# Kernel optimization log

Hardware: AMD Instinct MI355X
Metric: run time of the kernel (lower is better)

The kernel has to match this reference:

```python
import jax, jax.numpy as jnp
import numpy as np

B, S, HID = 1, 4096, 2048
NH, NKV, HD = 8, 4, 256
SCALING = 256.0 ** -0.5
SOFT_CAP = 50.0
WINDOW = 4096
ROPE_THETA = 10000.0
NEG = jnp.finfo(jnp.float32).min


def _build_mask():
    q = np.arange(S)[:, None]
    k = np.arange(S)[None, :]
    causal = k <= q
    windowed = (q - k) < WINDOW
    allowed = causal & windowed
    m = np.where(allowed, 0.0, np.finfo(np.float32).min).astype(np.float32)
    return jnp.asarray(m)[None, None]  # [1,1,S,S]


def setup_inputs() -> dict:
    key = jax.random.key(0)
    ks = jax.random.split(key, 5)
    scale = 0.02
    return {
        "hidden_states": jax.random.normal(ks[0], (B, S, HID), jnp.float32),
        "attention_mask": _build_mask(),
        "position_ids": jnp.arange(S, dtype=jnp.int64)[None, :],
        "wq": jax.random.normal(ks[1], (HID, NH * HD), jnp.float32) * scale,
        "wk": jax.random.normal(ks[2], (HID, NKV * HD), jnp.float32) * scale,
        "wv": jax.random.normal(ks[3], (HID, NKV * HD), jnp.float32) * scale,
        "wo": jax.random.normal(ks[4], (NH * HD, HID), jnp.float32) * scale,
    }


def _rope(position_ids):
    inv_freq = 1.0 / (ROPE_THETA ** (jnp.arange(0, HD, 2, dtype=jnp.float32) / HD))
    freqs = position_ids.astype(jnp.float32)[:, :, None] * inv_freq[None, None, :]  # [B,S,HD/2]
    emb = jnp.concatenate([freqs, freqs], axis=-1)  # [B,S,HD]
    return jnp.cos(emb), jnp.sin(emb)


def _rotate_half(x):
    x1, x2 = x[..., : HD // 2], x[..., HD // 2 :]
    return jnp.concatenate([-x2, x1], axis=-1)


def _attn(hidden_states, attention_mask, position_ids, wq, wk, wv, wo):
    bsz, q_len, _ = hidden_states.shape
    q = (hidden_states @ wq).reshape(bsz, q_len, NH, HD).transpose(0, 2, 1, 3)    # [B,NH,S,HD]
    k = (hidden_states @ wk).reshape(bsz, q_len, NKV, HD).transpose(0, 2, 1, 3)   # [B,NKV,S,HD]
    v = (hidden_states @ wv).reshape(bsz, q_len, NKV, HD).transpose(0, 2, 1, 3)
    cos, sin = _rope(position_ids)
    cos, sin = cos[:, None], sin[:, None]  # [B,1,S,HD]
    q = q * cos + _rotate_half(q) * sin
    k = k * cos + _rotate_half(k) * sin
    n_rep = NH // NKV
    k = jnp.repeat(k, n_rep, axis=1)  # [B,NH,S,HD]
    v = jnp.repeat(v, n_rep, axis=1)
    scores = jnp.einsum("bhqd,bhkd->bhqk", q, k) * SCALING
    scores = jnp.tanh(scores / SOFT_CAP) * SOFT_CAP
    scores = scores + attention_mask
    probs = jax.nn.softmax(scores.astype(jnp.float32), axis=-1).astype(q.dtype)
    out = jnp.einsum("bhqk,bhkd->bhqd", probs, v)  # [B,NH,S,HD]
    out = out.transpose(0, 2, 1, 3).reshape(bsz, q_len, NH * HD)
    return out @ wo


def reference(hidden_states, attention_mask, position_ids, wq, wk, wv, wo):
    return _attn(hidden_states, attention_mask, position_ids, wq, wk, wv, wo)
```

## Files before the change

### kernel.cpp

```cpp
#include <hip/hip_runtime.h>


#define SEQ 4096
#define HIDDEN 2048
#define NHEADS 8
#define HDIM 256

typedef unsigned short u16;
typedef __attribute__((ext_vector_type(8))) __bf16 bf16x8;
typedef __attribute__((ext_vector_type(4))) float f32x4;
typedef __attribute__((ext_vector_type(16))) float f32x16;

static __device__ inline u16 f2bf(float f) {
  union { float f; unsigned u; } x; x.f = f;
  unsigned r = x.u + 0x7FFFu + ((x.u >> 16) & 1u);
  return (u16)(r >> 16);
}
static __device__ inline float bf2f(u16 u) {
  union { unsigned u; float f; } x; x.u = ((unsigned)u) << 16;
  return x.f;
}

typedef __attribute__((address_space(1))) const unsigned int* gp_t;
typedef __attribute__((address_space(3))) unsigned int* lp_t;
static __device__ inline void load_lds16(const u16* g, u16* l) {
  __builtin_amdgcn_global_load_lds((gp_t)g, (lp_t)l, 16, 0, 0);
}


__global__ void convert_hs_kernel(const float* __restrict__ src, u16* __restrict__ dst) {
  int i = blockIdx.x * 256 + threadIdx.x;
  float4 v = ((const float4*)src)[i];
  ushort4 o;
  o.x = f2bf(v.x); o.y = f2bf(v.y); o.z = f2bf(v.z); o.w = f2bf(v.w);
  ((ushort4*)dst)[i] = o;
}

__global__ void transpose_w_kernel(const float* __restrict__ src, u16* __restrict__ dst,
                                   int K, int N) {
  __shared__ u16 tile[64][65];
  int n0 = blockIdx.x * 64, k0 = blockIdx.y * 64;
  int tid = threadIdx.x;
  for (int i = 0; i < 16; i++) {
    int idx = i * 256 + tid; int r = idx >> 6, c = idx & 63;
    tile[r][c] = f2bf(src[(size_t)(k0 + r) * N + n0 + c]);
  }
  __syncthreads();
  for (int i = 0; i < 16; i++) {
    int idx = i * 256 + tid; int r = idx >> 6, c = idx & 63;
    dst[(size_t)(n0 + r) * K + k0 + c] = tile[c][r];
  }
}

__global__ void rope_kernel(u16* qkv) {
  int idx = blockIdx.x * 256 + threadIdx.x;
  int s = idx / (12 * 128);
  int rem = idx - s * (12 * 128);
  int head = rem >> 7;
  int i = rem & 127;
  float inv = __expf(-(float)i * 0.0719557841560639f);
  float ang = (float)s * inv;
  float sn, cs;
  sincosf(ang, &sn, &cs);
  size_t base = (size_t)s * 4096 + head * 256 + i;
  float a = bf2f(qkv[base]);
  float b = bf2f(qkv[base + 128]);
  qkv[base]       = f2bf(a * cs - b * sn);
  qkv[base + 128] = f2bf(b * cs + a * sn);
}

__global__ void transpose_v_kernel(const u16* __restrict__ qkv, u16* __restrict__ vT) {
  __shared__ u16 tile[64][65];
  int d0 = blockIdx.x * 64, s0 = blockIdx.y * 64;
  int tid = threadIdx.x;
  for (int i = 0; i < 16; i++) {
    int idx = i * 256 + tid; int r = idx >> 6, c = idx & 63;
    tile[r][c] = qkv[(size_t)(s0 + r) * 4096 + 3072 + d0 + c];
  }
  __syncthreads();
  for (int i = 0; i < 16; i++) {
    int idx = i * 256 + tid; int r = idx >> 6, c = idx & 63;
    vT[(size_t)(d0 + r) * 4096 + s0 + c] = tile[c][r];
  }
}


template <bool OUT_F32>
__global__ __launch_bounds__(256, 2) void gemm_bf16_kernel(
    const u16* __restrict__ A, const u16* __restrict__ Bt, void* __restrict__ Cout,
    int M, int N, int K) {
  __shared__ __attribute__((aligned(16))) u16 As[128 * 64];
  __shared__ __attribute__((aligned(16))) u16 Bs[128 * 64];
  int tid = threadIdx.x;
  int wave = tid >> 6, lane = tid & 63;
  int lm = lane & 15, qd = lane >> 4;
  int m0 = blockIdx.y * 128, n0 = blockIdx.x * 128;
  int wm = (wave >> 1) * 64, wn = (wave & 1) * 64;

  f32x4 acc[4][4];
#pragma unroll
  for (int a = 0; a < 4; a++)
#pragma unroll
    for (int b = 0; b < 4; b++) acc[a][b] = (f32x4){0.f, 0.f, 0.f, 0.f};

  int srow = lane >> 3;
  int scol = (lane & 7) * 8;

  for (int kt = 0; kt < K; kt += 64) {
    __syncthreads();
#pragma unroll
    for (int t = 0; t < 4; t++) {
      int j = wave * 4 + t;
      int row = j * 8 + srow;
      load_lds16(A  + (size_t)(m0 + row) * K + kt + scol, As + j * 512);
      load_lds16(Bt + (size_t)(n0 + row) * K + kt + scol, Bs + j * 512);
    }
    __syncthreads();
#pragma unroll
    for (int kk = 0; kk < 2; kk++) {
      bf16x8 af[4], bfr[4];
#pragma unroll
      for (int mi = 0; mi < 4; mi++)
        af[mi] = *(const bf16x8*)&As[(wm + mi * 16 + lm) * 64 + kk * 32 + qd * 8];
#pragma unroll
      for (int ni = 0; ni < 4; ni++)
        bfr[ni] = *(const bf16x8*)&Bs[(wn + ni * 16 + lm) * 64 + kk * 32 + qd * 8];
#pragma unroll
      for (int mi = 0; mi < 4; mi++)
#pragma unroll
        for (int ni = 0; ni < 4; ni++)
          acc[mi][ni] = __builtin_amdgcn_mfma_f32_16x16x32_bf16(af[mi], bfr[ni],
                                                               acc[mi][ni], 0, 0, 0);
    }
  }
#pragma unroll
  for (int mi = 0; mi < 4; mi++) {
    int row = m0 + wm + mi * 16 + qd * 4;
#pragma unroll
    for (int ni = 0; ni < 4; ni++) {
      int col = n0 + wn + ni * 16 + lm;
#pragma unroll
      for (int r = 0; r < 4; r++) {
        float v = acc[mi][ni][r];
        if (OUT_F32) ((float*)Cout)[(size_t)(row + r) * N + col] = v;
        else         ((u16*)Cout)[(size_t)(row + r) * N + col] = f2bf(v);
      }
    }
  }
}


__global__ __launch_bounds__(256, 2) void flash_kernel(
    const u16* __restrict__ qkv, const u16* __restrict__ vT,
    u16* __restrict__ attn, float* __restrict__ PA, float* __restrict__ PB,
    float* __restrict__ lbuf ) {
  __shared__ __attribute__((aligned(16))) u16 Ks[64 * 256];
  __shared__ __attribute__((aligned(16))) u16 Vs[256 * 64];
  __shared__ __attribute__((aligned(16))) u16 Pl[64 * 64];

  int tid = threadIdx.x;
  int w = tid >> 6, lane = tid & 63;
  int l31 = lane & 31, hi = lane >> 5;
  int qhalf = w >> 1, kh = w & 1, dhalf = w & 1;

  int b = blockIdx.x;
  int r = b & 255;
  int h = r & 7;
  int pi = r >> 3;
  int kvh = h >> 1;
  int isA = (b < 256);
  int nseg = isA ? 2 : 1;

  int vlc = (lane & 7) ^ ((lane >> 3) & 7);
  int vro = lane >> 3;

  const u16* Kg  = qkv + 2048 + (size_t)kvh * 256;
  const u16* Vg0 = vT + (size_t)(kvh * 256) * 4096;

  bf16x8 ones;
#pragma unroll
  for (int e = 0; e < 8; e++) ones[e] = (__bf16)1.0f;

  for (int si = 0; si < nseg; si++) {
    int qt, k0, k1, mode;
    if (isA && si == 0) { qt = pi;      k0 = 0;       k1 = pi + 1;  mode = 0; }
    else if (isA)       { qt = 63 - pi; k0 = 0;       k1 = 31 - pi; mode = 1; }
    else                { qt = 63 - pi; k0 = 31 - pi; k1 = 64 - pi; mode = 2; }

    {
      const u16* Qg = qkv + (size_t)(qt * 64) * 4096 + h * 256;
#pragma unroll
      for (int s = 0; s < 8; s++) {
        int kr = (w * 8 + s) * 2 + hi;
        int klc = l31 ^ (kr & 31);
        load_lds16(Qg + (size_t)kr * 4096 + klc * 8, &Ks[(w * 8 + s) * 512]);
      }
    }
    __syncthreads();

    bf16x8 aq[16];
#pragma unroll
    for (int kc = 0; kc < 16; kc++)
      aq[kc] = *(const bf16x8*)&Ks[(qhalf * 32 + l31) * 256 +
                                   (((kc * 2 + hi) ^ l31) << 3)];
    __syncthreads();

    f32x16 ao[4];
#pragma unroll
    for (int g = 0; g < 4; g++) ao[g] = (f32x16)(0.f);
    f32x16 al = (f32x16)(0.f);

    for (int t = k0; t < k1; t++) {
      {
        const u16* Kt = Kg + (size_t)(t * 64) * 4096;
        const u16* Vt = Vg0 + t * 64;
#pragma unroll
        for (int s = 0; s < 8; s++) {
          int kr = (w * 8 + s) * 2 + hi;
          int klc = l31 ^ (kr & 31);
          load_lds16(Kt + (size_t)kr * 4096 + klc * 8, &Ks[(w * 8 + s) * 512]);
          int vr = (w * 8 + s) * 8 + vro;
          load_lds16(Vt + (size_t)vr * 4096 + vlc * 8, &Vs[(w * 8 + s) * 512]);
        }
      }
      __syncthreads();

      f32x16 se = (f32x16)(0.f);
      f32x16 so = (f32x16)(0.f);
#pragma unroll
      for (int kc = 0; kc < 8; kc++) {
        bf16x8 bk0 = *(const bf16x8*)&Ks[(kh * 32 + l31) * 256 +
                                         ((((2 * kc) * 2 + hi) ^ l31) << 3)];
        se = __builtin_amdgcn_mfma_f32_32x32x16_bf16(aq[2 * kc], bk0, se, 0, 0, 0);
        bf16x8 bk1 = *(const bf16x8*)&Ks[(kh * 32 + l31) * 256 +
                                         ((((2 * kc + 1) * 2 + hi) ^ l31) << 3)];
        so = __builtin_amdgcn_mfma_f32_32x32x16_bf16(aq[2 * kc + 1], bk1, so, 0, 0, 0);
      }
      f32x16 sacc = se + so;

      bool diag = (t == qt);
#pragma unroll
      for (int reg = 0; reg < 16; reg++) {
        int qa = 4 * hi + 8 * (reg >> 2) + (reg & 3);
        int q64 = qhalf * 32 + qa;
        int key64 = kh * 32 + l31;
        float x = sacc[reg] * 0.00125f;
        float x2 = x * x;
        float th = x * (1.f + x2 * (-0.33333333f + x2 * 0.13333333f));
        float p = exp2f(72.134752f * (th - 1.f));
        if (diag && key64 > q64) p = 0.f;
        Pl[q64 * 64 + (((key64 >> 3) ^ (q64 & 7)) << 3) + (key64 & 7)] = f2bf(p);
      }
      __syncthreads();

      bf16x8 ap[4];
#pragma unroll
      for (int kc = 0; kc < 4; kc++)
        ap[kc] = *(const bf16x8*)&Pl[(qhalf * 32 + l31) * 64 +
                                     (((kc * 2 + hi) ^ (l31 & 7)) << 3)];
#pragma unroll
      for (int g = 0; g < 4; g++) {
        int dd = dhalf * 128 + g * 32 + l31;
#pragma unroll
        for (int kc = 0; kc < 4; kc++) {
          bf16x8 bv = *(const bf16x8*)&Vs[dd * 64 +
                                          (((kc * 2 + hi) ^ (l31 & 7)) << 3)];
          ao[g] = __builtin_amdgcn_mfma_f32_32x32x16_bf16(ap[kc], bv, ao[g], 0, 0, 0);
        }
      }
#pragma unroll
      for (int kc = 0; kc < 4; kc++)
        al = __builtin_amdgcn_mfma_f32_32x32x16_bf16(ap[kc], ones, al, 0, 0, 0);

      __syncthreads();
    }

    if (mode == 0) {
      float inv_l[16];
#pragma unroll
      for (int reg = 0; reg < 16; reg++) inv_l[reg] = 1.f / al[reg];
      int qs = qt * 64 + qhalf * 32;
#pragma unroll
      for (int g = 0; g < 4; g++) {
        int col = h * 256 + dhalf * 128 + g * 32 + l31;
#pragma unroll
        for (int reg = 0; reg < 16; reg++) {
          int row = qs + 4 * hi + 8 * (reg >> 2) + (reg & 3);
          attn[(size_t)row * 2048 + col] = f2bf(ao[g][reg] * inv_l[reg]);
        }
      }
    } else {
      float* Pbuf = (mode == 1) ? PA : PB;
#pragma unroll
      for (int g = 0; g < 4; g++) {
        int col = dhalf * 128 + g * 32 + l31;
#pragma unroll
        for (int reg = 0; reg < 16; reg++) {
          int row = qhalf * 32 + 4 * hi + 8 * (reg >> 2) + (reg & 3);
          Pbuf[((size_t)r * 64 + row) * 256 + col] = ao[g][reg];
        }
      }
      if (dhalf == 0 && l31 == 0) {
        size_t lbase = (size_t)(r * 16 + (mode - 1)) * 2048 + 1536;
#pragma unroll
        for (int reg = 0; reg < 16; reg++) {
          int row = qhalf * 32 + 4 * hi + 8 * (reg >> 2) + (reg & 3);
          lbuf[lbase + row] = al[reg];
        }
      }
    }
  }
}

__global__ __launch_bounds__(256) void combine_kernel(
    const float* __restrict__ PA, const float* __restrict__ PB,
    const float* __restrict__ lbuf, u16* __restrict__ attn) {
  int p = blockIdx.x;
  int h = p & 7, pi = p >> 3;
  int qt2 = 63 - pi;
  int tid = threadIdx.x;
  int row = tid >> 2;
  int c0 = (tid & 3) * 64;
  float la = lbuf[(size_t)(p * 16) * 2048 + 1536 + row];
  float lb = lbuf[(size_t)(p * 16 + 1) * 2048 + 1536 + row];
  float inv = 1.f / (la + lb);
  size_t src = ((size_t)p * 64 + row) * 256 + c0;
  size_t dst = (size_t)(qt2 * 64 + row) * 2048 + h * 256 + c0;
#pragma unroll
  for (int c = 0; c < 64; c += 4) {
    float4 a = *(const float4*)&PA[src + c];
    float4 bb = *(const float4*)&PB[src + c];
    ushort4 o;
    o.x = f2bf((a.x + bb.x) * inv);
    o.y = f2bf((a.y + bb.y) * inv);
    o.z = f2bf((a.z + bb.z) * inv);
    o.w = f2bf((a.w + bb.w) * inv);
    *(ushort4*)&attn[dst + c] = o;
  }
}


extern "C" void kernel_launch(void* const* d_in, const int* in_sizes, int n_in,
                              void* d_out, int out_size, void* d_ws, size_t ws_size,
                              hipStream_t stream) {
  const float* hs = (const float*)d_in[0];
  const float* wq = (const float*)d_in[3];
  const float* wk = (const float*)d_in[4];
  const float* wv = (const float*)d_in[5];
  const float* wo = (const float*)d_in[6];
  float* out = (float*)d_out;

  char* ws = (char*)d_ws;
  u16* hsb    = (u16*)(ws);
  u16* wqkvT  = (u16*)(ws + 16777216);
  u16* woT    = (u16*)(ws + 33554432);
  u16* qkv    = (u16*)(ws + 41943040);
  u16* vT     = (u16*)(ws + 75497472);
  u16* attn   = (u16*)(ws + 83886080);
  float* PA   = (float*)(ws);
  float* PB   = (float*)(ws + 16777216);
  float* lbuf = (float*)(ws + 41943040);

  convert_hs_kernel<<<8192, 256, 0, stream>>>(hs, hsb);
  transpose_w_kernel<<<dim3(32, 32), 256, 0, stream>>>(wq, wqkvT, HIDDEN, 2048);
  transpose_w_kernel<<<dim3(16, 32), 256, 0, stream>>>(wk, wqkvT + (size_t)2048 * HIDDEN, HIDDEN, 1024);
  transpose_w_kernel<<<dim3(16, 32), 256, 0, stream>>>(wv, wqkvT + (size_t)3072 * HIDDEN, HIDDEN, 1024);
  transpose_w_kernel<<<dim3(32, 32), 256, 0, stream>>>(wo, woT, HIDDEN, 2048);

  gemm_bf16_kernel<false><<<dim3(32, 32), 256, 0, stream>>>(hsb, wqkvT, qkv, 4096, 4096, 2048);
  rope_kernel<<<24576, 256, 0, stream>>>(qkv);
  transpose_v_kernel<<<dim3(16, 64), 256, 0, stream>>>(qkv, vT);

  flash_kernel<<<512, 256, 0, stream>>>(qkv, vT, attn, PA, PB, lbuf);
  combine_kernel<<<256, 256, 0, stream>>>(PA, PB, lbuf, attn);
  gemm_bf16_kernel<true><<<dim3(16, 32), 256, 0, stream>>>(attn, woT, out, 4096, 2048, 2048);
}
```

Baseline: 482.6 us.

## Add 256x256-tile pipelined GEMM for the fused QKV projection

```diff
diff --git a/kernel.cpp b/kernel.cpp
--- a/kernel.cpp
+++ b/kernel.cpp
@@ -26,6 +26,8 @@
 static __device__ inline void load_lds16(const u16* g, u16* l) {
   __builtin_amdgcn_global_load_lds((gp_t)g, (lp_t)l, 16, 0, 0);
 }
+
+#define BARX() do { __builtin_amdgcn_s_barrier(); asm volatile("" ::: "memory"); } while (0)
 
 
 __global__ void convert_hs_kernel(const float* __restrict__ src, u16* __restrict__ dst) {
@@ -85,6 +87,110 @@
 }
 
 
+__global__ __launch_bounds__(512, 2) void gemm256_kernel(
+    const u16* __restrict__ A, const u16* __restrict__ Bt, u16* __restrict__ C,
+    int M, int N, int K) {
+  __shared__ __attribute__((aligned(16))) u16 lds[4][2][256 * 32];
+  int tid = threadIdx.x;
+  int wid = tid >> 6, lane = tid & 63;
+  int lm = lane & 15, kq = lane >> 4;
+  int wm = (wid >> 2) * 128, wn = (wid & 3) * 64;
+  int m0 = blockIdx.y * 256, n0 = blockIdx.x * 256;
+  int T = K >> 5;
+
+  int idx0 = tid, idx1 = 512 + tid;
+  int r0 = idx0 >> 2, c0 = idx0 & 3;
+  int r1 = idx1 >> 2, c1 = idx1 & 3;
+  const u16* gA0 = A  + (size_t)(m0 + r0) * K + ((c0 ^ (r0 & 3)) << 3);
+  const u16* gA1 = A  + (size_t)(m0 + r1) * K + ((c1 ^ (r1 & 3)) << 3);
+  const u16* gB0 = Bt + (size_t)(n0 + r0) * K + ((c0 ^ (r0 & 3)) << 3);
+  const u16* gB1 = Bt + (size_t)(n0 + r1) * K + ((c1 ^ (r1 & 3)) << 3);
+
+  f32x4 acc[8][4];
+#pragma unroll
+  for (int a = 0; a < 8; a++)
+#pragma unroll
+    for (int b = 0; b < 4; b++) acc[a][b] = (f32x4){0.f, 0.f, 0.f, 0.f};
+
+  int xsw = ((kq ^ (lm & 3)) << 3);
+
+#pragma unroll
+  for (int t = 0; t < 2; t++) {
+    int s = t & 3;
+    load_lds16(gA0 + t * 32, &lds[s][0][idx0 * 8]);
+    load_lds16(gA1 + t * 32, &lds[s][0][idx1 * 8]);
+    load_lds16(gB0 + t * 32, &lds[s][1][idx0 * 8]);
+    load_lds16(gB1 + t * 32, &lds[s][1][idx1 * 8]);
+  }
+  asm volatile("s_waitcnt vmcnt(4)" ::: "memory");
+  BARX();
+
+  for (int t = 0; t < T; ++t) {
+    const u16* As = &lds[t & 3][0][0];
+    const u16* Bs = &lds[t & 3][1][0];
+    int sn = (t + 2) & 3;
+    bool st = (t + 2) < T;
+
+    bf16x8 a0[4], bb[4];
+#pragma unroll
+    for (int f = 0; f < 4; f++)
+      a0[f] = *(const bf16x8*)&As[(wm + f * 16 + lm) * 32 + xsw];
+#pragma unroll
+    for (int f = 0; f < 4; f++)
+      bb[f] = *(const bf16x8*)&Bs[(wn + f * 16 + lm) * 32 + xsw];
+    if (st) {
+      load_lds16(gA0 + (t + 2) * 32, &lds[sn][0][idx0 * 8]);
+      load_lds16(gA1 + (t + 2) * 32, &lds[sn][0][idx1 * 8]);
+    }
+    BARX();
+    __builtin_amdgcn_s_setprio(1);
+#pragma unroll
+    for (int mi = 0; mi < 4; mi++)
+#pragma unroll
+      for (int ni = 0; ni < 4; ni++)
+        acc[mi][ni] = __builtin_amdgcn_mfma_f32_16x16x32_bf16(a0[mi], bb[ni],
+                                                             acc[mi][ni], 0, 0, 0);
+    __builtin_amdgcn_s_setprio(0);
+
+    bf16x8 a1[4];
+#pragma unroll
+    for (int f = 0; f < 4; f++)
+      a1[f] = *(const bf16x8*)&As[(wm + 64 + f * 16 + lm) * 32 + xsw];
+    if (st) {
+      load_lds16(gB0 + (t + 2) * 32, &lds[sn][1][idx0 * 8]);
+      load_lds16(gB1 + (t + 2) * 32, &lds[sn][1][idx1 * 8]);
+    }
+    BARX();
+    __builtin_amdgcn_s_setprio(1);
+#pragma unroll
+    for (int mi = 0; mi < 4; mi++)
+#pragma unroll
+      for (int ni = 0; ni < 4; ni++)
+        acc[4 + mi][ni] = __builtin_amdgcn_mfma_f32_16x16x32_bf16(a1[mi], bb[ni],
+                                                                 acc[4 + mi][ni], 0, 0, 0);
+    __builtin_amdgcn_s_setprio(0);
+
+    if (t < T - 1) {
+      if (st) asm volatile("s_waitcnt vmcnt(4)" ::: "memory");
+      else    asm volatile("s_waitcnt vmcnt(0)" ::: "memory");
+      BARX();
+    }
+  }
+
+#pragma unroll
+  for (int mi = 0; mi < 8; mi++) {
+    int row = m0 + wm + mi * 16 + kq * 4;
+#pragma unroll
+    for (int ni = 0; ni < 4; ni++) {
+      int col = n0 + wn + ni * 16 + lm;
+#pragma unroll
+      for (int r = 0; r < 4; r++)
+        C[(size_t)(row + r) * N + col] = f2bf(acc[mi][ni][r]);
+    }
+  }
+}
+
+
 template <bool OUT_F32>
 __global__ __launch_bounds__(256, 2) void gemm_bf16_kernel(
     const u16* __restrict__ A, const u16* __restrict__ Bt, void* __restrict__ Cout,
@@ -367,7 +473,7 @@
   transpose_w_kernel<<<dim3(16, 32), 256, 0, stream>>>(wv, wqkvT + (size_t)3072 * HIDDEN, HIDDEN, 1024);
   transpose_w_kernel<<<dim3(32, 32), 256, 0, stream>>>(wo, woT, HIDDEN, 2048);
 
-  gemm_bf16_kernel<false><<<dim3(32, 32), 256, 0, stream>>>(hsb, wqkvT, qkv, 4096, 4096, 2048);
+  gemm256_kernel<<<dim3(16, 16), 512, 0, stream>>>(hsb, wqkvT, qkv, 4096, 4096, 2048);
   rope_kernel<<<24576, 256, 0, stream>>>(qkv);
   transpose_v_kernel<<<dim3(16, 64), 256, 0, stream>>>(qkv, vT);
 
```

Result: no change. 475.2 us (-1.5%).

## Fuse prep kernels and add double-buffered 256x128 GEMM for QKV projection

Applied to the files above, without the earlier changes.

```diff
diff --git a/kernel.cpp b/kernel.cpp
--- a/kernel.cpp
+++ b/kernel.cpp
@@ -27,20 +27,30 @@
   __builtin_amdgcn_global_load_lds((gp_t)g, (lp_t)l, 16, 0, 0);
 }
 
-
-__global__ void convert_hs_kernel(const float* __restrict__ src, u16* __restrict__ dst) {
-  int i = blockIdx.x * 256 + threadIdx.x;
-  float4 v = ((const float4*)src)[i];
-  ushort4 o;
-  o.x = f2bf(v.x); o.y = f2bf(v.y); o.z = f2bf(v.z); o.w = f2bf(v.w);
-  ((ushort4*)dst)[i] = o;
-}
-
-__global__ void transpose_w_kernel(const float* __restrict__ src, u16* __restrict__ dst,
-                                   int K, int N) {
+#define BARX() do { __builtin_amdgcn_s_barrier(); asm volatile("" ::: "memory"); } while (0)
+
+
+__global__ void prep1_kernel(const float* __restrict__ hs, u16* __restrict__ hsb,
+                             const float* __restrict__ wq, const float* __restrict__ wk,
+                             const float* __restrict__ wv, const float* __restrict__ wo,
+                             u16* __restrict__ wqkvT, u16* __restrict__ woT) {
   __shared__ u16 tile[64][65];
-  int n0 = blockIdx.x * 64, k0 = blockIdx.y * 64;
-  int tid = threadIdx.x;
+  int bid = blockIdx.x, tid = threadIdx.x;
+  if (bid < 8192) {
+    int i = bid * 256 + tid;
+    float4 v = ((const float4*)hs)[i];
+    ushort4 o;
+    o.x = f2bf(v.x); o.y = f2bf(v.y); o.z = f2bf(v.z); o.w = f2bf(v.w);
+    ((ushort4*)hsb)[i] = o;
+    return;
+  }
+  int tb = bid - 8192;
+  const float* src; u16* dst; int N, n0, k0;
+  if (tb < 1024)      { src = wq; dst = wqkvT;                        N = 2048; n0 = (tb & 31) * 64; k0 = (tb >> 5) * 64; }
+  else if (tb < 1536) { int x = tb - 1024; src = wk; dst = wqkvT + (size_t)2048 * 2048; N = 1024; n0 = (x & 15) * 64; k0 = (x >> 4) * 64; }
+  else if (tb < 2048) { int x = tb - 1536; src = wv; dst = wqkvT + (size_t)3072 * 2048; N = 1024; n0 = (x & 15) * 64; k0 = (x >> 4) * 64; }
+  else                { int x = tb - 2048; src = wo; dst = woT;       N = 2048; n0 = (x & 31) * 64; k0 = (x >> 5) * 64; }
+  const int K = 2048;
   for (int i = 0; i < 16; i++) {
     int idx = i * 256 + tid; int r = idx >> 6, c = idx & 63;
     tile[r][c] = f2bf(src[(size_t)(k0 + r) * N + n0 + c]);
@@ -52,27 +62,31 @@
   }
 }
 
-__global__ void rope_kernel(u16* qkv) {
-  int idx = blockIdx.x * 256 + threadIdx.x;
-  int s = idx / (12 * 128);
-  int rem = idx - s * (12 * 128);
-  int head = rem >> 7;
-  int i = rem & 127;
-  float inv = __expf(-(float)i * 0.0719557841560639f);
-  float ang = (float)s * inv;
-  float sn, cs;
-  sincosf(ang, &sn, &cs);
-  size_t base = (size_t)s * 4096 + head * 256 + i;
-  float a = bf2f(qkv[base]);
-  float b = bf2f(qkv[base + 128]);
-  qkv[base]       = f2bf(a * cs - b * sn);
-  qkv[base + 128] = f2bf(b * cs + a * sn);
-}
-
-__global__ void transpose_v_kernel(const u16* __restrict__ qkv, u16* __restrict__ vT) {
+
+__global__ void prep2_kernel(u16* __restrict__ qkv, u16* __restrict__ vT) {
   __shared__ u16 tile[64][65];
-  int d0 = blockIdx.x * 64, s0 = blockIdx.y * 64;
-  int tid = threadIdx.x;
+  int bid = blockIdx.x, tid = threadIdx.x;
+  if (bid < 2048) {
+    int idx = bid * 256 + tid;
+    int s = idx >> 7;
+    int i = idx & 127;
+    float inv = __expf(-(float)i * 0.0719557841560639f);
+    float ang = (float)s * inv;
+    float sn, cs;
+    sincosf(ang, &sn, &cs);
+    size_t rowb = (size_t)s * 4096;
+#pragma unroll
+    for (int hh = 0; hh < 12; hh++) {
+      size_t base = rowb + hh * 256 + i;
+      float a = bf2f(qkv[base]);
+      float b = bf2f(qkv[base + 128]);
+      qkv[base]       = f2bf(a * cs - b * sn);
+      qkv[base + 128] = f2bf(b * cs + a * sn);
+    }
+    return;
+  }
+  int x = bid - 2048;
+  int d0 = (x & 15) * 64, s0 = (x >> 4) * 64;
   for (int i = 0; i < 16; i++) {
     int idx = i * 256 + tid; int r = idx >> 6, c = idx & 63;
     tile[r][c] = qkv[(size_t)(s0 + r) * 4096 + 3072 + d0 + c];
@@ -81,6 +95,81 @@
   for (int i = 0; i < 16; i++) {
     int idx = i * 256 + tid; int r = idx >> 6, c = idx & 63;
     vT[(size_t)(d0 + r) * 4096 + s0 + c] = tile[c][r];
+  }
+}
+
+
+__global__ __launch_bounds__(512, 4) void gemm_mn_kernel(
+    const u16* __restrict__ A, const u16* __restrict__ Bt, u16* __restrict__ C,
+    int M, int N, int K) {
+  __shared__ __attribute__((aligned(16))) u16 As[2][256 * 32];
+  __shared__ __attribute__((aligned(16))) u16 Bs[2][128 * 32];
+  int tid = threadIdx.x;
+  int wid = tid >> 6, lane = tid & 63;
+  int lm = lane & 15, kq = lane >> 4;
+  int wm = (wid >> 1) * 64, wn = (wid & 1) * 64;
+  int m0 = blockIdx.y * 256, n0 = blockIdx.x * 128;
+  int T = K >> 5;
+
+  int r0 = tid >> 2, c0 = tid & 3;
+  int csw = ((c0 ^ (r0 & 3)) << 3);
+  const u16* gA0 = A  + (size_t)(m0 + r0) * K + csw;
+  const u16* gA1 = A  + (size_t)(m0 + 128 + r0) * K + csw;
+  const u16* gB0 = Bt + (size_t)(n0 + r0) * K + csw;
+
+  f32x4 acc[4][4];
+#pragma unroll
+  for (int a = 0; a < 4; a++)
+#pragma unroll
+    for (int b = 0; b < 4; b++) acc[a][b] = (f32x4){0.f, 0.f, 0.f, 0.f};
+
+  int xsw = ((kq ^ (lm & 3)) << 3);
+
+  load_lds16(gA0, &As[0][tid * 8]);
+  load_lds16(gA1, &As[0][(512 + tid) * 8]);
+  load_lds16(gB0, &Bs[0][tid * 8]);
+  asm volatile("s_waitcnt vmcnt(0)" ::: "memory");
+  BARX();
+
+  for (int t = 0; t < T; ++t) {
+    int cur = t & 1;
+    if (t + 1 < T) {
+      int nb = 1 - cur;
+      load_lds16(gA0 + (t + 1) * 32, &As[nb][tid * 8]);
+      load_lds16(gA1 + (t + 1) * 32, &As[nb][(512 + tid) * 8]);
+      load_lds16(gB0 + (t + 1) * 32, &Bs[nb][tid * 8]);
+    }
+    bf16x8 af[4], bfr[4];
+#pragma unroll
+    for (int f = 0; f < 4; f++)
+      af[f] = *(const bf16x8*)&As[cur][(wm + f * 16 + lm) * 32 + xsw];
+#pragma unroll
+    for (int f = 0; f < 4; f++)
+      bfr[f] = *(const bf16x8*)&Bs[cur][(wn + f * 16 + lm) * 32 + xsw];
+    __builtin_amdgcn_s_setprio(1);
+#pragma unroll
+    for (int mi = 0; mi < 4; mi++)
+#pragma unroll
+      for (int ni = 0; ni < 4; ni++)
+        acc[mi][ni] = __builtin_amdgcn_mfma_f32_16x16x32_bf16(af[mi], bfr[ni],
+                                                             acc[mi][ni], 0, 0, 0);
+    __builtin_amdgcn_s_setprio(0);
+    if (t + 1 < T) {
+      asm volatile("s_waitcnt vmcnt(0)" ::: "memory");
+      BARX();
+    }
+  }
+
+#pragma unroll
+  for (int mi = 0; mi < 4; mi++) {
+    int row = m0 + wm + mi * 16 + kq * 4;
+#pragma unroll
+    for (int ni = 0; ni < 4; ni++) {
+      int col = n0 + wn + ni * 16 + lm;
+#pragma unroll
+      for (int r = 0; r < 4; r++)
+        C[(size_t)(row + r) * N + col] = f2bf(acc[mi][ni][r]);
+    }
   }
 }
 
@@ -361,16 +450,9 @@
   float* PB   = (float*)(ws + 16777216);
   float* lbuf = (float*)(ws + 41943040);
 
-  convert_hs_kernel<<<8192, 256, 0, stream>>>(hs, hsb);
-  transpose_w_kernel<<<dim3(32, 32), 256, 0, stream>>>(wq, wqkvT, HIDDEN, 2048);
-  transpose_w_kernel<<<dim3(16, 32), 256, 0, stream>>>(wk, wqkvT + (size_t)2048 * HIDDEN, HIDDEN, 1024);
-  transpose_w_kernel<<<dim3(16, 32), 256, 0, stream>>>(wv, wqkvT + (size_t)3072 * HIDDEN, HIDDEN, 1024);
-  transpose_w_kernel<<<dim3(32, 32), 256, 0, stream>>>(wo, woT, HIDDEN, 2048);
-
-  gemm_bf16_kernel<false><<<dim3(32, 32), 256, 0, stream>>>(hsb, wqkvT, qkv, 4096, 4096, 2048);
-  rope_kernel<<<24576, 256, 0, stream>>>(qkv);
-  transpose_v_kernel<<<dim3(16, 64), 256, 0, stream>>>(qkv, vT);
-
+  prep1_kernel<<<11264, 256, 0, stream>>>(hs, hsb, wq, wk, wv, wo, wqkvT, woT);
+  gemm_mn_kernel<<<dim3(32, 16), 512, 0, stream>>>(hsb, wqkvT, qkv, 4096, 4096, 2048);
+  prep2_kernel<<<3072, 256, 0, stream>>>(qkv, vT);
   flash_kernel<<<512, 256, 0, stream>>>(qkv, vT, attn, PA, PB, lbuf);
   combine_kernel<<<256, 256, 0, stream>>>(PA, PB, lbuf, attn);
   gemm_bf16_kernel<true><<<dim3(16, 32), 256, 0, stream>>>(attn, woT, out, 4096, 2048, 2048);
```

Result: faster. 453.5 us (-6.0%).
